# Optimization experiments

Hardware: AMD Instinct MI355X
Metric: run time of the kernel (lower is better)

## Reference

```python
import jax, jax.numpy as jnp
import numpy as np

B = 4096       # batch of query embeddings
E = 512        # embedding_size
C = 2000       # num_classes
PROXIES = 32   # imprinted weight vectors per class
P = C * PROXIES  # 64000 total stacked weight rows
EPS = 1e-12    # torch F.normalize eps


def _l2_normalize(x):
    # F.normalize(x, p=2, dim=1): divide by norm clamped to eps
    n = jnp.linalg.norm(x, axis=1, keepdims=True)
    return x / jnp.maximum(n, EPS)


def setup_inputs() -> dict:
    key = jax.random.key(0)
    k1, k2 = jax.random.split(key)
    data = jax.random.normal(k1, (B, E), dtype=jnp.float32)
    w1 = jax.random.normal(k2, (P, E), dtype=jnp.float32)
    segment_ids = jnp.arange(P, dtype=jnp.int32)  # raw row index; class id derived in reference
    return {"data": data, "w1": w1, "segment_ids": segment_ids}


def reference(data, w1, segment_ids):
    # class id of each stacked weight row (contiguous blocks, as torch vstack([*w1s]))
    seg = (segment_ids * C) // P  # == idx // PROXIES, shape [P]
    # normalize: input data at forward time; weights were l2-normalized at imprint time
    d = _l2_normalize(data)   # [B, E]
    w = _l2_normalize(w1)     # [P, E]
    # x = w1 @ data.T : per-proxy activations  [P, B]
    x = jnp.einsum('pe,be->pb', w, d)
    # per-class max over each class's ragged proxy block -> [C, B]
    y = jax.ops.segment_max(x, seg, num_segments=C)
    return y
```

## Files before the change

kernel.cpp:

```cpp
#include <hip/hip_runtime.h>

#define B_Q   4096
#define E_DIM 512
#define N_C   2000
#define N_P   64000

#define BM 256
#define BN 256

typedef int i32x4 __attribute__((ext_vector_type(4)));

__device__ __forceinline__ void async_ld16(const void* g, void* l) {
  __builtin_amdgcn_global_load_lds(
      (const __attribute__((address_space(1))) void*)g,
      (__attribute__((address_space(3))) void*)l,
      16, 0, 0);
}

__global__ __launch_bounds__(128) void normq_kernel(
    const float* __restrict__ w1, const float* __restrict__ data,
    signed char* __restrict__ wq, signed char* __restrict__ dq,
    float* __restrict__ wsc, float* __restrict__ dsc)
{
  int row = blockIdx.x;
  const float* in; signed char* outq; float* sc;
  if (row < N_P) { in = w1;   outq = wq; sc = wsc; }
  else           { in = data; outq = dq; sc = dsc; row -= N_P; }
  const int tid = threadIdx.x;
  const float4 v = *(const float4*)(in + (size_t)row * E_DIM + tid * 4);
  float ss = v.x*v.x + v.y*v.y + v.z*v.z + v.w*v.w;
  float am = fmaxf(fmaxf(fabsf(v.x), fabsf(v.y)), fmaxf(fabsf(v.z), fabsf(v.w)));
  #pragma unroll
  for (int s = 1; s < 64; s <<= 1) {
    ss += __shfl_xor(ss, s);
    am = fmaxf(am, __shfl_xor(am, s));
  }
  __shared__ float pss[2], pam[2];
  if ((tid & 63) == 0) { pss[tid >> 6] = ss; pam[tid >> 6] = am; }
  __syncthreads();
  const float inv = 1.0f / fmaxf(sqrtf(pss[0] + pss[1]), 1e-12f);
  const float m   = fmaxf(fmaxf(pam[0], pam[1]) * inv, 1e-20f);
  const float qs  = 127.0f / m * inv;
  char4 o;
  o.x = (signed char)__float2int_rn(v.x * qs);
  o.y = (signed char)__float2int_rn(v.y * qs);
  o.z = (signed char)__float2int_rn(v.z * qs);
  o.w = (signed char)__float2int_rn(v.w * qs);
  *(char4*)(outq + (size_t)row * E_DIM + tid * 4) = o;
  if (tid == 0) sc[row] = m * (1.0f / 127.0f);
}

#define WAITV(N) asm volatile("s_waitcnt vmcnt(" #N ")" ::: "memory")
#define SBAR     asm volatile("s_barrier" ::: "memory")
#define NOPS     do {} while (0)

#define STAGE_A(BUF,H,KOFF) do { \
  async_ld16(gA + (KOFF)*128 + (H)*64,         smem + (BUF)*32768 + (H)*16384 + sdst); \
  async_ld16(gA + 65536 + (KOFF)*128 + (H)*64, smem + (BUF)*32768 + (H)*16384 + sdst + 8192); \
} while(0)

#define STAGE_B(BUF,H,KOFF) do { \
  async_ld16(gB + (KOFF)*128 + (H)*64,         smem + 65536 + (BUF)*32768 + (H)*16384 + sdst); \
  async_ld16(gB + 65536 + (KOFF)*128 + (H)*64, smem + 65536 + (BUF)*32768 + (H)*16384 + sdst + 8192); \
} while(0)

#define RDA(S,BUF,H,MH) do { \
  a##S##_0 = *(const i32x4*)(pa + (BUF)*32768 + (H)*16384 + ((MH)*4+0)*1024); \
  a##S##_1 = *(const i32x4*)(pa + (BUF)*32768 + (H)*16384 + ((MH)*4+1)*1024); \
  a##S##_2 = *(const i32x4*)(pa + (BUF)*32768 + (H)*16384 + ((MH)*4+2)*1024); \
  a##S##_3 = *(const i32x4*)(pa + (BUF)*32768 + (H)*16384 + ((MH)*4+3)*1024); \
} while(0)

#define RDB01(S,BUF,H) do { \
  b##S##_0 = *(const i32x4*)(pb + (BUF)*32768 + (H)*16384 +    0); \
  b##S##_1 = *(const i32x4*)(pb + (BUF)*32768 + (H)*16384 + 1024); \
} while(0)

#define RDB23(S,BUF,H) do { \
  b##S##_2 = *(const i32x4*)(pb + (BUF)*32768 + (H)*16384 + 2048); \
  b##S##_3 = *(const i32x4*)(pb + (BUF)*32768 + (H)*16384 + 3072); \
} while(0)

#define MM(AS,BS,MH,m,n) \
  acc[(MH)*4+m][n] = __builtin_amdgcn_mfma_i32_16x16x64_i8( \
      a##AS##_##m, b##BS##_##n, acc[(MH)*4+m][n], 0, 0, 0)

#define MFMA16(AS,BS,MH) do { \
  MM(AS,BS,MH,0,0); MM(AS,BS,MH,0,1); MM(AS,BS,MH,0,2); MM(AS,BS,MH,0,3); \
  MM(AS,BS,MH,1,0); MM(AS,BS,MH,1,1); MM(AS,BS,MH,1,2); MM(AS,BS,MH,1,3); \
  MM(AS,BS,MH,2,0); MM(AS,BS,MH,2,1); MM(AS,BS,MH,2,2); MM(AS,BS,MH,2,3); \
  MM(AS,BS,MH,3,0); MM(AS,BS,MH,3,1); MM(AS,BS,MH,3,2); MM(AS,BS,MH,3,3); \
} while(0)

#define SGB(M,N) __builtin_amdgcn_sched_group_barrier(M, N, 0)
#define ILV6 do { \
  SGB(0x8,2); SGB(0x100,1); SGB(0x8,2); SGB(0x100,1); \
  SGB(0x8,2); SGB(0x100,1); SGB(0x8,2); SGB(0x100,1); \
  SGB(0x8,2); SGB(0x100,1); SGB(0x8,2); SGB(0x100,1); \
  SGB(0x8,4); \
} while(0)
#define ILV4 do { \
  SGB(0x8,2); SGB(0x100,1); SGB(0x8,2); SGB(0x100,1); \
  SGB(0x8,2); SGB(0x100,1); SGB(0x8,2); SGB(0x100,1); \
  SGB(0x8,8); \
} while(0)

#define PHX(AS,BS,MH, STAGE, WAIT, TAIL, ILV) do { \
  STAGE; \
  WAIT; \
  SBAR; \
  asm volatile("s_waitcnt lgkmcnt(0)" ::: "memory"); \
  __builtin_amdgcn_sched_barrier(0); \
  __builtin_amdgcn_s_setprio(1); \
  MFMA16(AS,BS,MH); \
  TAIL; \
  ILV; \
  __builtin_amdgcn_s_setprio(0); \
  SBAR; \
} while(0)

#define IIBLK(K1,K2,K3) do { \
  PHX(0,0,0, STAGE_A(1,1,K1), WAITV(6), RDA(1,0,0,1); RDB01(1,0,1), ILV6); \
  PHX(1,0,1, STAGE_B(1,1,K1), NOPS,     RDA(0,0,1,0); RDB23(1,0,1), ILV6); \
  PHX(0,1,0, STAGE_A(0,0,K2), WAITV(6), RDA(1,0,1,1); RDB01(0,1,0), ILV6); \
  PHX(1,1,1, STAGE_B(0,0,K2), NOPS,     RDA(0,1,0,0); RDB23(0,1,0), ILV6); \
  PHX(0,0,0, STAGE_A(0,1,K2), WAITV(6), RDA(1,1,0,1); RDB01(1,1,1), ILV6); \
  PHX(1,0,1, STAGE_B(0,1,K2), NOPS,     RDA(0,1,1,0); RDB23(1,1,1), ILV6); \
  PHX(0,1,0, STAGE_A(1,0,K3), WAITV(6), RDA(1,1,1,1); RDB01(0,0,0), ILV6); \
  PHX(1,1,1, STAGE_B(1,0,K3), NOPS,     RDA(0,0,0,0); RDB23(0,0,0), ILV6); \
} while(0)

__global__ __launch_bounds__(512, 2) void gemm_max_kernel(
    const signed char* __restrict__ wq,
    const signed char* __restrict__ dq,
    const float* __restrict__ wsc,
    const float* __restrict__ dsc,
    float* __restrict__ out)
{
  extern __shared__ char smem[];

  const int tid  = threadIdx.x;
  const int lane = tid & 63;
  const int wid  = tid >> 6;
  const int wr   = wid >> 2;
  const int wc   = wid & 3;

  const int bid  = blockIdx.x;
  const int wgid = (bid & 7) * 500 + (bid >> 3);
  const int rowb = wgid >> 4;
  const int colb = wgid & 15;
  const int rowBase = rowb * BM;
  const int colBase = colb * BN;

  const int srow = tid >> 2;
  const int gch  = (tid & 3) ^ ((tid >> 3) & 3);
  const signed char* gA = wq + (size_t)(rowBase + srow) * E_DIM + gch * 16;
  const signed char* gB = dq + (size_t)(colBase + srow) * E_DIM + gch * 16;
  const int sdst = tid * 16;

  const int r   = lane & 15;
  const int kg  = lane >> 4;
  const int swz = (kg ^ ((r >> 1) & 3)) * 16;
  const char* pa = smem + (wr * 128 + r) * 64 + swz;
  const char* pb = smem + 65536 + (wc * 64 + r) * 64 + swz;

  i32x4 acc[8][4];
  #pragma unroll
  for (int m = 0; m < 8; ++m)
    #pragma unroll
    for (int n = 0; n < 4; ++n)
      acc[m][n] = (i32x4){0, 0, 0, 0};

  i32x4 a0_0, a0_1, a0_2, a0_3, a1_0, a1_1, a1_2, a1_3;
  i32x4 b0_0, b0_1, b0_2, b0_3, b1_0, b1_1, b1_2, b1_3;

  STAGE_A(0,0,0); STAGE_B(0,0,0);
  STAGE_A(0,1,0); STAGE_B(0,1,0);
  STAGE_A(1,0,1); STAGE_B(1,0,1);
  WAITV(8);
  SBAR;
  RDA(0,0,0,0);
  RDB01(0,0,0);
  RDB23(0,0,0);

  IIBLK(1,2,3);
  PHX(0,0,0, STAGE_A(1,1,3), WAITV(6), RDA(1,0,0,1); RDB01(1,0,1), ILV6);
  PHX(1,0,1, STAGE_B(1,1,3), NOPS,     RDA(0,0,1,0); RDB23(1,0,1), ILV6);
  PHX(0,1,0, NOPS,           WAITV(4), RDA(1,0,1,1); RDB01(0,1,0), ILV6);
  PHX(1,1,1, NOPS,           NOPS,     RDA(0,1,0,0); RDB23(0,1,0), ILV6);
  PHX(0,0,0, NOPS,           WAITV(0), RDA(1,1,0,1); RDB01(1,1,1), ILV6);
  PHX(1,0,1, NOPS,           NOPS,     RDA(0,1,1,0); RDB23(1,1,1), ILV6);
  PHX(0,1,0, NOPS,           NOPS,     RDA(1,1,1,1),               ILV4);
  PHX(1,1,1, NOPS,           NOPS,     NOPS,                       NOPS);

  float wsv[8][4];
  {
    const float* wscp = wsc + rowBase + wr * 128 + kg * 4;
    #pragma unroll
    for (int m = 0; m < 8; ++m)
      #pragma unroll
      for (int j = 0; j < 4; ++j)
        wsv[m][j] = wscp[m * 16 + j];
  }
  float dv[4];
  {
    const float* dscp = dsc + colBase + wc * 64 + r;
    #pragma unroll
    for (int n = 0; n < 4; ++n) dv[n] = dscp[n * 16];
  }
  const int classBase = rowb * 8 + wr * 4;
  #pragma unroll
  for (int q = 0; q < 4; ++q) {
    #pragma unroll
    for (int n = 0; n < 4; ++n) {
      float pm = -3.4e38f;
      #pragma unroll
      for (int j = 0; j < 4; ++j)
        pm = fmaxf(pm, fmaxf((float)acc[2*q][n][j]   * wsv[2*q][j],
                             (float)acc[2*q+1][n][j] * wsv[2*q+1][j]));
      pm = fmaxf(pm, __shfl_xor(pm, 16));
      pm = fmaxf(pm, __shfl_xor(pm, 32));
      if (lane < 16)
        out[(size_t)(classBase + q) * B_Q + colBase + wc * 64 + n * 16 + r]
            = pm * dv[n];
    }
  }
}

extern "C" void kernel_launch(void* const* d_in, const int* in_sizes, int n_in,
                              void* d_out, int out_size, void* d_ws, size_t ws_size,
                              hipStream_t stream) {
  const float* data = (const float*)d_in[0];
  const float* w1   = (const float*)d_in[1];
  float* out = (float*)d_out;

  signed char* wq = (signed char*)d_ws;
  signed char* dq = wq + (size_t)N_P * E_DIM;
  float* wsc = (float*)(dq + (size_t)B_Q * E_DIM);
  float* dsc = wsc + N_P;

  (void)hipFuncSetAttribute((const void*)gemm_max_kernel,
      hipFuncAttributeMaxDynamicSharedMemorySize, 131072);

  normq_kernel<<<N_P + B_Q, 128, 0, stream>>>(w1, data, wq, dq, wsc, dsc);
  gemm_max_kernel<<<4000, 512, 131072, stream>>>(wq, dq, wsc, dsc, out);
}
```

Before: 191.6 us.

## Shrink GEMM tiles to 128x128 with simpler double-buffered K loop

Cuts the int8 GEMM+segment-max tile from 256x256 to 128x128 and drops from 8 to 4 waves per block. The complex interleaved schedule (sched_group_barrier, split A/B staging) becomes a plain double-buffered loop using 32KB of static LDS. Four blocks per CU should raise occupancy and latency hiding. In exchange each block reuses operands less, so global and LDS traffic per MFMA rises, and the hand-tuned MFMA/LDS interleave is gone.

```diff
diff --git a/kernel.cpp b/kernel.cpp
--- a/kernel.cpp
+++ b/kernel.cpp
@@ -5,8 +5,8 @@
 #define N_C   2000
 #define N_P   64000
 
-#define BM 256
-#define BN 256
+#define BM 128
+#define BN 128
 
 typedef int i32x4 __attribute__((ext_vector_type(4)));
 
@@ -51,104 +51,72 @@
 }
 
 #define WAITV(N) asm volatile("s_waitcnt vmcnt(" #N ")" ::: "memory")
+#define LGKM0    asm volatile("s_waitcnt lgkmcnt(0)" ::: "memory")
 #define SBAR     asm volatile("s_barrier" ::: "memory")
 #define NOPS     do {} while (0)
 
-#define STAGE_A(BUF,H,KOFF) do { \
-  async_ld16(gA + (KOFF)*128 + (H)*64,         smem + (BUF)*32768 + (H)*16384 + sdst); \
-  async_ld16(gA + 65536 + (KOFF)*128 + (H)*64, smem + (BUF)*32768 + (H)*16384 + sdst + 8192); \
-} while(0)
-
-#define STAGE_B(BUF,H,KOFF) do { \
-  async_ld16(gB + (KOFF)*128 + (H)*64,         smem + 65536 + (BUF)*32768 + (H)*16384 + sdst); \
-  async_ld16(gB + 65536 + (KOFF)*128 + (H)*64, smem + 65536 + (BUF)*32768 + (H)*16384 + sdst + 8192); \
-} while(0)
-
-#define RDA(S,BUF,H,MH) do { \
-  a##S##_0 = *(const i32x4*)(pa + (BUF)*32768 + (H)*16384 + ((MH)*4+0)*1024); \
-  a##S##_1 = *(const i32x4*)(pa + (BUF)*32768 + (H)*16384 + ((MH)*4+1)*1024); \
-  a##S##_2 = *(const i32x4*)(pa + (BUF)*32768 + (H)*16384 + ((MH)*4+2)*1024); \
-  a##S##_3 = *(const i32x4*)(pa + (BUF)*32768 + (H)*16384 + ((MH)*4+3)*1024); \
-} while(0)
-
-#define RDB01(S,BUF,H) do { \
-  b##S##_0 = *(const i32x4*)(pb + (BUF)*32768 + (H)*16384 +    0); \
-  b##S##_1 = *(const i32x4*)(pb + (BUF)*32768 + (H)*16384 + 1024); \
-} while(0)
-
-#define RDB23(S,BUF,H) do { \
-  b##S##_2 = *(const i32x4*)(pb + (BUF)*32768 + (H)*16384 + 2048); \
-  b##S##_3 = *(const i32x4*)(pb + (BUF)*32768 + (H)*16384 + 3072); \
-} while(0)
-
-#define MM(AS,BS,MH,m,n) \
-  acc[(MH)*4+m][n] = __builtin_amdgcn_mfma_i32_16x16x64_i8( \
-      a##AS##_##m, b##BS##_##n, acc[(MH)*4+m][n], 0, 0, 0)
-
-#define MFMA16(AS,BS,MH) do { \
-  MM(AS,BS,MH,0,0); MM(AS,BS,MH,0,1); MM(AS,BS,MH,0,2); MM(AS,BS,MH,0,3); \
-  MM(AS,BS,MH,1,0); MM(AS,BS,MH,1,1); MM(AS,BS,MH,1,2); MM(AS,BS,MH,1,3); \
-  MM(AS,BS,MH,2,0); MM(AS,BS,MH,2,1); MM(AS,BS,MH,2,2); MM(AS,BS,MH,2,3); \
-  MM(AS,BS,MH,3,0); MM(AS,BS,MH,3,1); MM(AS,BS,MH,3,2); MM(AS,BS,MH,3,3); \
-} while(0)
-
-#define SGB(M,N) __builtin_amdgcn_sched_group_barrier(M, N, 0)
-#define ILV6 do { \
-  SGB(0x8,2); SGB(0x100,1); SGB(0x8,2); SGB(0x100,1); \
-  SGB(0x8,2); SGB(0x100,1); SGB(0x8,2); SGB(0x100,1); \
-  SGB(0x8,2); SGB(0x100,1); SGB(0x8,2); SGB(0x100,1); \
-  SGB(0x8,4); \
-} while(0)
-#define ILV4 do { \
-  SGB(0x8,2); SGB(0x100,1); SGB(0x8,2); SGB(0x100,1); \
-  SGB(0x8,2); SGB(0x100,1); SGB(0x8,2); SGB(0x100,1); \
-  SGB(0x8,8); \
-} while(0)
-
-#define PHX(AS,BS,MH, STAGE, WAIT, TAIL, ILV) do { \
+#define STAGE_A(BUF,KOFF) do { \
+  async_ld16(gA + (KOFF)*64,         smem + (BUF)*8192 + sdst); \
+  async_ld16(gA + 32768 + (KOFF)*64, smem + (BUF)*8192 + sdst + 4096); \
+} while(0)
+
+#define STAGE_B(BUF,KOFF) do { \
+  async_ld16(gB + (KOFF)*64,         smem + 16384 + (BUF)*8192 + sdst); \
+  async_ld16(gB + 32768 + (KOFF)*64, smem + 16384 + (BUF)*8192 + sdst + 4096); \
+} while(0)
+
+#define RD(BUF) do { \
+  fa0 = *(const i32x4*)(pa + (BUF)*8192 +    0); \
+  fa1 = *(const i32x4*)(pa + (BUF)*8192 + 1024); \
+  fa2 = *(const i32x4*)(pa + (BUF)*8192 + 2048); \
+  fa3 = *(const i32x4*)(pa + (BUF)*8192 + 3072); \
+  fb0 = *(const i32x4*)(pb + (BUF)*8192 +    0); \
+  fb1 = *(const i32x4*)(pb + (BUF)*8192 + 1024); \
+  fb2 = *(const i32x4*)(pb + (BUF)*8192 + 2048); \
+  fb3 = *(const i32x4*)(pb + (BUF)*8192 + 3072); \
+} while(0)
+
+#define MM(m,n) \
+  acc[m][n] = __builtin_amdgcn_mfma_i32_16x16x64_i8(fa##m, fb##n, acc[m][n], 0, 0, 0)
+
+#define MFMA16 do { \
+  MM(0,0); MM(0,1); MM(0,2); MM(0,3); \
+  MM(1,0); MM(1,1); MM(1,2); MM(1,3); \
+  MM(2,0); MM(2,1); MM(2,2); MM(2,3); \
+  MM(3,0); MM(3,1); MM(3,2); MM(3,3); \
+} while(0)
+
+#define ITER(BUF, STAGE, WAIT) do { \
+  RD(BUF); \
+  LGKM0; \
+  SBAR; \
   STAGE; \
   WAIT; \
   SBAR; \
-  asm volatile("s_waitcnt lgkmcnt(0)" ::: "memory"); \
-  __builtin_amdgcn_sched_barrier(0); \
   __builtin_amdgcn_s_setprio(1); \
-  MFMA16(AS,BS,MH); \
-  TAIL; \
-  ILV; \
+  MFMA16; \
   __builtin_amdgcn_s_setprio(0); \
-  SBAR; \
-} while(0)
-
-#define IIBLK(K1,K2,K3) do { \
-  PHX(0,0,0, STAGE_A(1,1,K1), WAITV(6), RDA(1,0,0,1); RDB01(1,0,1), ILV6); \
-  PHX(1,0,1, STAGE_B(1,1,K1), NOPS,     RDA(0,0,1,0); RDB23(1,0,1), ILV6); \
-  PHX(0,1,0, STAGE_A(0,0,K2), WAITV(6), RDA(1,0,1,1); RDB01(0,1,0), ILV6); \
-  PHX(1,1,1, STAGE_B(0,0,K2), NOPS,     RDA(0,1,0,0); RDB23(0,1,0), ILV6); \
-  PHX(0,0,0, STAGE_A(0,1,K2), WAITV(6), RDA(1,1,0,1); RDB01(1,1,1), ILV6); \
-  PHX(1,0,1, STAGE_B(0,1,K2), NOPS,     RDA(0,1,1,0); RDB23(1,1,1), ILV6); \
-  PHX(0,1,0, STAGE_A(1,0,K3), WAITV(6), RDA(1,1,1,1); RDB01(0,0,0), ILV6); \
-  PHX(1,1,1, STAGE_B(1,0,K3), NOPS,     RDA(0,0,0,0); RDB23(0,0,0), ILV6); \
-} while(0)
-
-__global__ __launch_bounds__(512, 2) void gemm_max_kernel(
+} while(0)
+
+__global__ __launch_bounds__(256, 4) void gemm_max_kernel(
     const signed char* __restrict__ wq,
     const signed char* __restrict__ dq,
     const float* __restrict__ wsc,
     const float* __restrict__ dsc,
     float* __restrict__ out)
 {
-  extern __shared__ char smem[];
+  __shared__ __align__(16) char smem[32768];
 
   const int tid  = threadIdx.x;
   const int lane = tid & 63;
   const int wid  = tid >> 6;
-  const int wr   = wid >> 2;
-  const int wc   = wid & 3;
+  const int wr   = wid >> 1;
+  const int wc   = wid & 1;
 
   const int bid  = blockIdx.x;
-  const int wgid = (bid & 7) * 500 + (bid >> 3);
-  const int rowb = wgid >> 4;
-  const int colb = wgid & 15;
+  const int wgid = (bid & 7) * 2000 + (bid >> 3);
+  const int rowb = wgid >> 5;
+  const int colb = wgid & 31;
   const int rowBase = rowb * BM;
   const int colBase = colb * BN;
 
@@ -161,46 +129,39 @@
   const int r   = lane & 15;
   const int kg  = lane >> 4;
   const int swz = (kg ^ ((r >> 1) & 3)) * 16;
-  const char* pa = smem + (wr * 128 + r) * 64 + swz;
-  const char* pb = smem + 65536 + (wc * 64 + r) * 64 + swz;
-
-  i32x4 acc[8][4];
+  const char* pa = smem + (wr * 64 + r) * 64 + swz;
+  const char* pb = smem + 16384 + (wc * 64 + r) * 64 + swz;
+
+  i32x4 acc[4][4];
   #pragma unroll
-  for (int m = 0; m < 8; ++m)
+  for (int m = 0; m < 4; ++m)
     #pragma unroll
     for (int n = 0; n < 4; ++n)
       acc[m][n] = (i32x4){0, 0, 0, 0};
 
-  i32x4 a0_0, a0_1, a0_2, a0_3, a1_0, a1_1, a1_2, a1_3;
-  i32x4 b0_0, b0_1, b0_2, b0_3, b1_0, b1_1, b1_2, b1_3;
-
-  STAGE_A(0,0,0); STAGE_B(0,0,0);
-  STAGE_A(0,1,0); STAGE_B(0,1,0);
-  STAGE_A(1,0,1); STAGE_B(1,0,1);
-  WAITV(8);
+  i32x4 fa0, fa1, fa2, fa3, fb0, fb1, fb2, fb3;
+
+  STAGE_A(0,0); STAGE_B(0,0);
+  STAGE_A(1,1); STAGE_B(1,1);
+  WAITV(4);
   SBAR;
-  RDA(0,0,0,0);
-  RDB01(0,0,0);
-  RDB23(0,0,0);
-
-  IIBLK(1,2,3);
-  PHX(0,0,0, STAGE_A(1,1,3), WAITV(6), RDA(1,0,0,1); RDB01(1,0,1), ILV6);
-  PHX(1,0,1, STAGE_B(1,1,3), NOPS,     RDA(0,0,1,0); RDB23(1,0,1), ILV6);
-  PHX(0,1,0, NOPS,           WAITV(4), RDA(1,0,1,1); RDB01(0,1,0), ILV6);
-  PHX(1,1,1, NOPS,           NOPS,     RDA(0,1,0,0); RDB23(0,1,0), ILV6);
-  PHX(0,0,0, NOPS,           WAITV(0), RDA(1,1,0,1); RDB01(1,1,1), ILV6);
-  PHX(1,0,1, NOPS,           NOPS,     RDA(0,1,1,0); RDB23(1,1,1), ILV6);
-  PHX(0,1,0, NOPS,           NOPS,     RDA(1,1,1,1),               ILV4);
-  PHX(1,1,1, NOPS,           NOPS,     NOPS,                       NOPS);
-
-  float wsv[8][4];
+
+  ITER(0, STAGE_A(0,2); STAGE_B(0,2), WAITV(4));
+  ITER(1, STAGE_A(1,3); STAGE_B(1,3), WAITV(4));
+  ITER(0, STAGE_A(0,4); STAGE_B(0,4), WAITV(4));
+  ITER(1, STAGE_A(1,5); STAGE_B(1,5), WAITV(4));
+  ITER(0, STAGE_A(0,6); STAGE_B(0,6), WAITV(4));
+  ITER(1, STAGE_A(1,7); STAGE_B(1,7), WAITV(4));
+  ITER(0, NOPS,                       WAITV(0));
+  ITER(1, NOPS,                       NOPS);
+
+  float wsv[4][4];
   {
-    const float* wscp = wsc + rowBase + wr * 128 + kg * 4;
-    #pragma unroll
-    for (int m = 0; m < 8; ++m)
-      #pragma unroll
-      for (int j = 0; j < 4; ++j)
-        wsv[m][j] = wscp[m * 16 + j];
+    #pragma unroll
+    for (int m = 0; m < 4; ++m) {
+      const float4 w4 = *(const float4*)(wsc + rowBase + wr * 64 + m * 16 + kg * 4);
+      wsv[m][0] = w4.x; wsv[m][1] = w4.y; wsv[m][2] = w4.z; wsv[m][3] = w4.w;
+    }
   }
   float dv[4];
   {
@@ -208,9 +169,9 @@
     #pragma unroll
     for (int n = 0; n < 4; ++n) dv[n] = dscp[n * 16];
   }
-  const int classBase = rowb * 8 + wr * 4;
+  const int classBase = rowb * 4 + wr * 2;
   #pragma unroll
-  for (int q = 0; q < 4; ++q) {
+  for (int q = 0; q < 2; ++q) {
     #pragma unroll
     for (int n = 0; n < 4; ++n) {
       float pm = -3.4e38f;
@@ -239,9 +200,6 @@
   float* wsc = (float*)(dq + (size_t)B_Q * E_DIM);
   float* dsc = wsc + N_P;
 
-  (void)hipFuncSetAttribute((const void*)gemm_max_kernel,
-      hipFuncAttributeMaxDynamicSharedMemorySize, 131072);
-
   normq_kernel<<<N_P + B_Q, 128, 0, stream>>>(w1, data, wq, dq, wsc, dsc);
-  gemm_max_kernel<<<4000, 512, 131072, stream>>>(wq, dq, wsc, dsc, out);
-}
+  gemm_max_kernel<<<(N_P / BM) * (B_Q / BN), 256, 0, stream>>>(wq, dq, wsc, dsc, out);
+}
```

New measurement: 185.1 us. 3.4% less time.
